# Kernel optimization log

Measured on AMD Instinct MI355X. Metric: run time of the kernel, lower is better.

## Reference

```python
import jax, jax.numpy as jnp
import numpy as np

B, L = 2, 2048
D_MODEL = 1024; D_STATE = 128; D_CONV = 4; EXPAND = 2; HEADDIM = 64
D_HALF = D_MODEL // 2
D_INNER = EXPAND * D_HALF           # 1024
NHEADS = D_INNER // HEADDIM         # 16
CONV_DIM = D_INNER + 2 * D_STATE    # 1280 (x, B, C share the depthwise conv)
D_IN_PROJ = 2 * D_INNER + 2 * D_STATE + NHEADS  # 2320 (z, xBC, dt)
EPS = 1e-5


def _rmsnorm(x, w):
    return x * jax.lax.rsqrt(jnp.mean(x * x, axis=-1, keepdims=True) + EPS) * w


def _mamba2(u, in_w, conv_w, conv_b, dt_bias, A_log, D, gnorm_w, outp_w):
    """Mamba2 block (ngroups=1, rmsnorm gated, no proj biases), u: [b,l,D_HALF]."""
    b, l, _ = u.shape
    zxbcdt = u @ in_w.T                                # [b,l,D_IN_PROJ]
    z = zxbcdt[..., :D_INNER]
    xBC = zxbcdt[..., D_INNER:D_INNER + CONV_DIM]
    dt = zxbcdt[..., D_INNER + CONV_DIM:]              # [b,l,h]
    # causal depthwise conv1d (kernel D_CONV) + silu
    xp = jnp.pad(xBC, ((0, 0), (D_CONV - 1, 0), (0, 0)))
    conv = conv_b + sum(xp[:, k:k + l, :] * conv_w[:, k] for k in range(D_CONV))
    xBC = jax.nn.silu(conv)
    x = xBC[..., :D_INNER]
    Bm = xBC[..., D_INNER:D_INNER + D_STATE]           # [b,l,n]
    Cm = xBC[..., D_INNER + D_STATE:]                  # [b,l,n]
    dt = jax.nn.softplus(dt + dt_bias)                 # [b,l,h]
    A = -jnp.exp(A_log)                                # [h]
    xh = x.reshape(b, l, NHEADS, HEADDIM)              # [b,l,h,p]
    dA = jnp.exp(dt * A)                               # [b,l,h]
    dtx = dt[..., None] * xh                           # [b,l,h,p]

    def step(h, inp):
        dA_t, dtx_t, B_t, C_t = inp
        h = dA_t[:, :, None, None] * h + jnp.einsum('bhp,bn->bhpn', dtx_t, B_t)
        return h, jnp.einsum('bhpn,bn->bhp', h, C_t)

    h0 = jnp.zeros((b, NHEADS, HEADDIM, D_STATE), u.dtype)
    xs = (jnp.moveaxis(dA, 1, 0), jnp.moveaxis(dtx, 1, 0),
          jnp.moveaxis(Bm, 1, 0), jnp.moveaxis(Cm, 1, 0))
    _, ys = jax.lax.scan(step, h0, xs)                 # ys: [l,b,h,p]
    y = jnp.moveaxis(ys, 0, 1) + xh * D[None, None, :, None]
    y = y.reshape(b, l, D_INNER) * jax.nn.silu(z)      # gate, then gated RMSNorm
    y = _rmsnorm(y, gnorm_w)
    return y @ outp_w.T                                # [b,l,D_HALF]


def _forward(x, norm_w, op_w, op_b,
             f_in_w, f_conv_w, f_conv_b, f_dt_bias, f_A_log, f_D, f_gnorm_w, f_outp_w,
             b_in_w, b_conv_w, b_conv_b, b_dt_bias, b_A_log, b_D, b_gnorm_w, b_outp_w):
    xn = _rmsnorm(x, norm_w)
    x_f, x_b = xn[..., :D_HALF], xn[..., D_HALF:]
    out_f = _mamba2(x_f, f_in_w, f_conv_w, f_conv_b, f_dt_bias, f_A_log, f_D, f_gnorm_w, f_outp_w)
    out_b = jnp.flip(
        _mamba2(jnp.flip(x_b, 1), b_in_w, b_conv_w, b_conv_b, b_dt_bias, b_A_log, b_D, b_gnorm_w, b_outp_w), 1)
    out = jnp.concatenate([out_f, out_b], axis=-1) @ op_w.T + op_b
    return x + out


def _mamba_params(key, prefix):
    k = jax.random.split(key, 5)
    return {
        prefix + 'in_w': jax.random.normal(k[0], (D_IN_PROJ, D_HALF), jnp.float32) * 0.02,
        prefix + 'conv_w': jax.random.normal(k[1], (CONV_DIM, D_CONV), jnp.float32) * 0.2,
        prefix + 'conv_b': jnp.zeros((CONV_DIM,), jnp.float32),
        prefix + 'dt_bias': jax.random.normal(k[2], (NHEADS,), jnp.float32) * 0.1,
        prefix + 'A_log': jnp.log(jax.random.uniform(k[3], (NHEADS,), jnp.float32, 1.0, 16.0)),
        prefix + 'D': jnp.ones((NHEADS,), jnp.float32),
        prefix + 'gnorm_w': jnp.ones((D_INNER,), jnp.float32),
        prefix + 'outp_w': jax.random.normal(k[4], (D_HALF, D_INNER), jnp.float32) * 0.02,
    }


def setup_inputs():
    key = jax.random.key(0)
    k = jax.random.split(key, 4)
    inp = {
        'x': jax.random.normal(k[0], (B, L, D_MODEL), jnp.float32),
        'norm_w': jnp.ones((D_MODEL,), jnp.float32),
        'op_w': jax.random.normal(k[1], (D_MODEL, D_MODEL), jnp.float32) * 0.02,
        'op_b': jnp.zeros((D_MODEL,), jnp.float32),
    }
    inp.update(_mamba_params(k[2], 'f_'))
    inp.update(_mamba_params(k[3], 'b_'))
    return inp


def reference(x, norm_w, op_w, op_b,
              f_in_w, f_conv_w, f_conv_b, f_dt_bias, f_A_log, f_D, f_gnorm_w, f_outp_w,
              b_in_w, b_conv_w, b_conv_b, b_dt_bias, b_A_log, b_D, b_gnorm_w, b_outp_w):
    return _forward(x, norm_w, op_w, op_b,
                    f_in_w, f_conv_w, f_conv_b, f_dt_bias, f_A_log, f_D, f_gnorm_w, f_outp_w,
                    b_in_w, b_conv_w, b_conv_b, b_dt_bias, b_A_log, b_D, b_gnorm_w, b_outp_w)
```

## Files before the change

### kernel.cpp

```cpp
#include <hip/hip_runtime.h>
#include <math.h>

#define L_SEQ   2048
#define NBATCH  2
#define DMODEL  1024
#define DHALF   512
#define DINNER  1024
#define DSTATE  128
#define NHEADS  16
#define HEADDIM 64
#define CONVDIM 1280
#define DINPROJ 2320
#define ROWS    4096
#define NPADIN  2432

#define QCH     64
#define NCH     (L_SEQ / QCH)

typedef __attribute__((ext_vector_type(8))) short bf16x8;
typedef __attribute__((ext_vector_type(4))) float f32x4;

union US8 { uint4 q; unsigned short s[8]; };
union US4 { uint2 q; unsigned short s[4]; };

__device__ __forceinline__ float siluf(float v){ return v / (1.f + expf(-v)); }
__device__ __forceinline__ float softplusf(float v){ return v > 20.f ? v : log1pf(expf(v)); }
__device__ __forceinline__ unsigned short f2bf(float f){
  union { float f; unsigned u; } x; x.f = f;
  unsigned r = (x.u + 0x7fffu + ((x.u >> 16) & 1u)) >> 16;
  return (unsigned short)r;
}
__device__ __forceinline__ float bf2f(unsigned short u){
  union { unsigned u; float f; } x; x.u = ((unsigned)u) << 16; return x.f;
}
__device__ __forceinline__ void gload16(const void* g, void* l){
  __builtin_amdgcn_global_load_lds((const __attribute__((address_space(1))) void*)g,
                                   (__attribute__((address_space(3))) void*)l, 16, 0, 0);
}
__device__ __forceinline__ int kx(int row){ return ((row ^ (row >> 3)) & 7) << 3; }

__device__ __forceinline__ float blockReduceSum256(float v, float* red){
  #pragma unroll
  for (int o = 32; o > 0; o >>= 1) v += __shfl_xor(v, o);
  int wid = threadIdx.x >> 6, lane = threadIdx.x & 63;
  if (lane == 0) red[wid] = v;
  __syncthreads();
  return red[0] + red[1] + red[2] + red[3];
}

__global__ void rmsnorm_split_kernel(const float* __restrict__ x, const float* __restrict__ nw,
                                     unsigned short* __restrict__ uf, unsigned short* __restrict__ ub){
  __shared__ float red[4];
  int row = blockIdx.x;
  int tid = threadIdx.x;
  float4 v4 = *(const float4*)(x + (size_t)row*DMODEL + tid*4);
  float ss = v4.x*v4.x + v4.y*v4.y + v4.z*v4.z + v4.w*v4.w;
  ss = blockReduceSum256(ss, red);
  float scale = rsqrtf(ss * (1.f/DMODEL) + 1e-5f);
  int t = row & (L_SEQ-1);
  int fliprow = (row ^ t) | (L_SEQ-1-t);
  float4 w4 = *(const float4*)(nw + tid*4);
  US4 o;
  o.s[0] = f2bf(v4.x*scale*w4.x);
  o.s[1] = f2bf(v4.y*scale*w4.y);
  o.s[2] = f2bf(v4.z*scale*w4.z);
  o.s[3] = f2bf(v4.w*scale*w4.w);
  int d = tid*4;
  if (d < DHALF) *(uint2*)&uf[(size_t)row*DHALF + d] = o.q;
  else           *(uint2*)&ub[(size_t)fliprow*DHALF + (d - DHALF)] = o.q;
}

__global__ void wconv_all_kernel(const float* __restrict__ s0, const float* __restrict__ s1,
                                 const float* __restrict__ s2, const float* __restrict__ s3,
                                 const float* __restrict__ s4,
                                 unsigned short* __restrict__ d0, unsigned short* __restrict__ d1,
                                 unsigned short* __restrict__ d2, unsigned short* __restrict__ d3,
                                 unsigned short* __restrict__ d4){
  const int S01 = NPADIN*DHALF;
  const int S23 = DHALF*DINNER;
  const int S4  = DMODEL*DMODEL;
  int idx = (blockIdx.x*256 + threadIdx.x)*4;
  const float* s; unsigned short* d; int pad_rows = 0;
  if (idx < S01){ s = s0; d = d0; pad_rows = DINPROJ; }
  else if ((idx -= S01) < S01){ s = s1; d = d1; pad_rows = DINPROJ; }
  else if ((idx -= S01) < S23){ s = s2; d = d2; }
  else if ((idx -= S23) < S23){ s = s3; d = d3; }
  else if ((idx -= S23) < S4){ s = s4; d = d4; }
  else return;
  US4 o;
  if (pad_rows && (idx >> 9) >= pad_rows){
    o.s[0] = o.s[1] = o.s[2] = o.s[3] = 0;
  } else {
    float4 v = *(const float4*)&s[idx];
    o.s[0] = f2bf(v.x); o.s[1] = f2bf(v.y); o.s[2] = f2bf(v.z); o.s[3] = f2bf(v.w);
  }
  *(uint2*)&d[idx] = o.q;
}

template<int TM>
__global__ __launch_bounds__(256) void gemm_bf16_t(
    const unsigned short* __restrict__ A0, const unsigned short* __restrict__ A1, int lda,
    const unsigned short* __restrict__ W0, const unsigned short* __restrict__ W1,
    float* __restrict__ Cf, int ldc,
    const float* __restrict__ bias, const float* __restrict__ res,
    unsigned short* __restrict__ O0a, unsigned short* __restrict__ O0b, int ld0,
    unsigned short* __restrict__ O1a, unsigned short* __restrict__ O1b, int n1, int ld1,
    float* __restrict__ O2a, float* __restrict__ O2b, int n2, int ld2,
    int coff1, int flip1,
    int M, int Nreal, int K){
  constexpr int MI = TM/32;
  __shared__ unsigned short As[2][TM*32];
  __shared__ unsigned short Bs[2][128*32];
  int bid = (blockIdx.z*gridDim.y + blockIdx.y)*gridDim.x + blockIdx.x;
  int nwg = gridDim.x*gridDim.y*gridDim.z;
  int s = bid;
  if ((nwg & 7) == 0){
    int cpx = nwg >> 3;
    s = (bid & 7)*cpx + (bid >> 3);
  }
  int bx = s % gridDim.x;
  int tmp = s / gridDim.x;
  int by = tmp % gridDim.y;
  int dir = tmp / gridDim.y;

  const unsigned short* A = dir ? A1 : A0;
  const unsigned short* W = dir ? W1 : W0;
  unsigned short* O0 = dir ? O0b : O0a;
  unsigned short* O1 = dir ? O1b : O1a;
  float* O2 = dir ? O2b : O2a;
  int coff = dir ? coff1 : 0;
  int flip = dir ? flip1 : 0;

  int bm = by*TM, bn = bx*128;
  int tid = threadIdx.x;
  int lane = tid & 63;
  int wave = tid >> 6;
  int wm = (wave >> 1) * (TM/2), wn = (wave & 1) * 64;
  int l15 = lane & 15, lhi = lane >> 4;
  f32x4 acc[MI][4];
  #pragma unroll
  for (int i = 0; i < MI; i++)
    #pragma unroll
    for (int j = 0; j < 4; j++)
      acc[i][j] = (f32x4){0.f,0.f,0.f,0.f};

  auto stage = [&](int bufi, int k0){
    #pragma unroll
    for (int f = tid; f < TM*4; f += 256){
      int row = f >> 2, c8 = (f & 3) * 8;
      gload16(A + (size_t)(bm+row)*lda + k0 + c8, &As[bufi][f*8]);
    }
    #pragma unroll
    for (int f = tid; f < 512; f += 256){
      int row = f >> 2, c8 = (f & 3) * 8;
      gload16(W + (size_t)(bn+row)*K + k0 + c8, &Bs[bufi][f*8]);
    }
  };

  stage(0, 0);
  __syncthreads();
  int cur = 0;
  for (int k0 = 0; k0 < K; k0 += 32){
    if (k0 + 32 < K) stage(cur ^ 1, k0 + 32);
    bf16x8 af[MI], bfr[4];
    #pragma unroll
    for (int i = 0; i < MI; i++)
      af[i] = *(const bf16x8*)&As[cur][(wm + i*16 + l15)*32 + lhi*8];
    #pragma unroll
    for (int j = 0; j < 4; j++)
      bfr[j] = *(const bf16x8*)&Bs[cur][(wn + j*16 + l15)*32 + lhi*8];
    #pragma unroll
    for (int i = 0; i < MI; i++)
      #pragma unroll
      for (int j = 0; j < 4; j++)
        acc[i][j] = __builtin_amdgcn_mfma_f32_16x16x32_bf16(af[i], bfr[j], acc[i][j], 0, 0, 0);
    __syncthreads();
    cur ^= 1;
  }
  #pragma unroll
  for (int i = 0; i < MI; i++){
    #pragma unroll
    for (int r = 0; r < 4; r++){
      int m = bm + wm + i*16 + lhi*4 + r;
      int mo = m;
      if (flip){ int t = m & (L_SEQ-1); mo = (m ^ t) | (L_SEQ-1-t); }
      #pragma unroll
      for (int j = 0; j < 4; j++){
        int n = bn + wn + j*16 + l15;
        if (n < Nreal){
          float v = acc[i][j][r];
          if (bias) v += bias[n];
          if (res)  v += res[(size_t)mo*ldc + coff + n];
          if (Cf)            Cf[(size_t)mo*ldc + coff + n] = v;
          else if (n < n1)   O0[(size_t)mo*ld0 + coff + n] = f2bf(v);
          else if (n < n2)   O1[(size_t)mo*ld1 + (n - n1)] = f2bf(v);
          else               O2[(size_t)mo*ld2 + (n - n2)] = v;
        }
      }
    }
  }
}

__global__ void conv_silu_kernel(const unsigned short* __restrict__ xbcf, const unsigned short* __restrict__ xbcb,
                                 const float* __restrict__ cwf, const float* __restrict__ cbf,
                                 const float* __restrict__ cwb, const float* __restrict__ cbb,
                                 unsigned short* __restrict__ cvf, unsigned short* __restrict__ cvb){
  int row = blockIdx.x;
  int tid = threadIdx.x;
  int dir = tid >= 160;
  int slot = tid - dir*160;
  const unsigned short* xbc = dir ? xbcb : xbcf;
  const float* cw = dir ? cwb : cwf;
  const float* cb = dir ? cbb : cbf;
  unsigned short* cv = dir ? cvb : cvf;
  int t = row & (L_SEQ-1);
  int c0 = slot*8;
  const unsigned short* base = xbc + (size_t)row*CONVDIM + c0;
  US8 u3, u2, u1, u0;
  u3.q = *(const uint4*)base;
  u2.q = (t >= 1) ? *(const uint4*)(base - CONVDIM)   : (uint4){0,0,0,0};
  u1.q = (t >= 2) ? *(const uint4*)(base - 2*CONVDIM) : (uint4){0,0,0,0};
  u0.q = (t >= 3) ? *(const uint4*)(base - 3*CONVDIM) : (uint4){0,0,0,0};
  US8 o;
  #pragma unroll
  for (int j = 0; j < 8; j++){
    float4 w = *(const float4*)&cw[(c0+j)*4];
    float v = cb[c0+j];
    v += bf2f(u3.s[j])*w.w + bf2f(u2.s[j])*w.z + bf2f(u1.s[j])*w.y + bf2f(u0.s[j])*w.x;
    o.s[j] = f2bf(siluf(v));
  }
  *(uint4*)&cv[(size_t)row*CONVDIM + c0] = o.q;
}

__global__ void dtcum_kernel(const float* __restrict__ drf, const float* __restrict__ drb,
                             const float* __restrict__ dbf, const float* __restrict__ alf,
                             const float* __restrict__ dbb, const float* __restrict__ alb,
                             float* __restrict__ dtf, float* __restrict__ dtb,
                             float* __restrict__ acs){
  int tid = threadIdx.x;
  int wid = blockIdx.x*4 + (tid >> 6);
  int tau = tid & 63;
  int c = wid & 31, dbh = wid >> 5;
  int h = dbh & 15, b = (dbh >> 4) & 1, dir = dbh >> 5;
  const float* dr = dir ? drb : drf;
  size_t row = (size_t)b*L_SEQ + c*QCH + tau;
  float raw = dr[row*NHEADS + h];
  float bias = (dir ? dbb : dbf)[h];
  float dtv = softplusf(raw + bias);
  float a = -expf((dir ? alb : alf)[h]);
  (dir ? dtb : dtf)[row*NHEADS + h] = dtv;
  float v = dtv * a;
  #pragma unroll
  for (int off = 1; off < 64; off <<= 1){
    float u = __shfl_up(v, off);
    if (tau >= off) v += u;
  }
  acs[(size_t)dbh*L_SEQ + c*QCH + tau] = v;
}

__global__ __launch_bounds__(256) void gemm_g_kernel(
    const unsigned short* __restrict__ cvf, const unsigned short* __restrict__ cvb,
    float* __restrict__ G){
  int c = blockIdx.x, db = blockIdx.y;
  int b = db & 1, dir = db >> 1;
  const unsigned short* cv = dir ? cvb : cvf;
  float* Gp = G + ((size_t)(db*32 + c))*4096;
  int tid = threadIdx.x, lane = tid & 63, w = tid >> 6;
  int l15 = lane & 15, lhi = lane >> 4;
  __shared__ unsigned short sB[64*128];
  __shared__ unsigned short sC[64*128];
  size_t r0 = (size_t)b*L_SEQ + (size_t)c*QCH;
  #pragma unroll
  for (int k = 0; k < 4; k++){
    int cid = k*256 + tid;
    int row = cid >> 4, slot = cid & 15;
    US8 ub, uc;
    ub.q = *(const uint4*)&cv[(r0+row)*CONVDIM + DINNER + slot*8];
    uc.q = *(const uint4*)&cv[(r0+row)*CONVDIM + DINNER + DSTATE + slot*8];
    *(uint4*)&sB[row*128 + (slot*8 ^ kx(row))] = ub.q;
    *(uint4*)&sC[row*128 + (slot*8 ^ kx(row))] = uc.q;
  }
  __syncthreads();
  int t0 = w*16;
  bf16x8 af[4];
  #pragma unroll
  for (int ks = 0; ks < 4; ks++){
    int r = t0 + l15;
    af[ks] = *(const bf16x8*)&sC[r*128 + ((ks*32 + lhi*8) ^ kx(r))];
  }
  f32x4 acc[4];
  #pragma unroll
  for (int j = 0; j < 4; j++) acc[j] = (f32x4){0.f,0.f,0.f,0.f};
  #pragma unroll
  for (int j = 0; j < 4; j++){
    #pragma unroll
    for (int ks = 0; ks < 4; ks++){
      int r = j*16 + l15;
      bf16x8 wf = *(const bf16x8*)&sB[r*128 + ((ks*32 + lhi*8) ^ kx(r))];
      acc[j] = __builtin_amdgcn_mfma_f32_16x16x32_bf16(af[ks], wf, acc[j], 0, 0, 0);
    }
  }
  #pragma unroll
  for (int j = 0; j < 4; j++)
    #pragma unroll
    for (int r = 0; r < 4; r++)
      Gp[(t0 + lhi*4 + r)*64 + j*16 + l15] = acc[j][r];
}

__global__ __launch_bounds__(256) void intra_kernel(
    const unsigned short* __restrict__ cvf, const unsigned short* __restrict__ cvb,
    const float* __restrict__ dtf, const float* __restrict__ dtb,
    const float* __restrict__ acs, const float* __restrict__ G,
    float* __restrict__ yf, float* __restrict__ yb,
    unsigned short* __restrict__ S16f, unsigned short* __restrict__ S16b){
  int c = blockIdx.x, dbh = blockIdx.y;
  int h = dbh & 15, b = (dbh >> 4) & 1, dir = dbh >> 5;
  const unsigned short* cv = dir ? cvb : cvf;
  const float* dtp = dir ? dtb : dtf;
  float* y = dir ? yb : yf;
  unsigned short* S16 = dir ? S16b : S16f;
  const float* Gp = G + ((size_t)((dir*2+b)*32 + c))*4096;
  int tid = threadIdx.x, lane = tid & 63, w = tid >> 6;
  int l15 = lane & 15, lhi = lane >> 4;

  __shared__ unsigned short sGh [64*64];
  __shared__ unsigned short sDxT[64*64];
  __shared__ unsigned short sBwT[128*64];
  __shared__ float a_sh[QCH], dt_sh[QCH];

  size_t r0 = (size_t)b*L_SEQ + (size_t)c*QCH;
  if (tid < 64){
    a_sh[tid]  = acs[(size_t)dbh*L_SEQ + c*QCH + tid];
    dt_sh[tid] = dtp[(r0 + tid)*NHEADS + h];
  }
  __syncthreads();
  float a63 = a_sh[63];
  #pragma unroll
  for (int k = 0; k < 2; k++){
    int cid = k*256 + tid;
    int s = cid >> 3, p0 = (cid & 7)*8;
    US8 u; u.q = *(const uint4*)&cv[(r0+s)*CONVDIM + h*HEADDIM + p0];
    float d = dt_sh[s];
    #pragma unroll
    for (int j = 0; j < 8; j++){
      int p = p0 + j;
      sDxT[p*64 + (s ^ kx(p))] = f2bf(bf2f(u.s[j]) * d);
    }
  }
  #pragma unroll
  for (int k = 0; k < 4; k++){
    int cid = k*256 + tid;
    int s = cid >> 4, n0 = (cid & 15)*8;
    US8 u; u.q = *(const uint4*)&cv[(r0+s)*CONVDIM + DINNER + n0];
    float wv = expf(a63 - a_sh[s]);
    #pragma unroll
    for (int j = 0; j < 8; j++){
      int n = n0 + j;
      sBwT[n*64 + (s ^ kx(n))] = f2bf(bf2f(u.s[j]) * wv);
    }
  }
  #pragma unroll
  for (int k = 0; k < 4; k++){
    int f = k*256 + tid;
    int t = f >> 4, s0 = (f & 15)*4;
    float4 g = *(const float4*)&Gp[t*64 + s0];
    float at = a_sh[t];
    float v0 = (s0+0 <= t) ? g.x*expf(at - a_sh[s0+0]) : 0.f;
    float v1 = (s0+1 <= t) ? g.y*expf(at - a_sh[s0+1]) : 0.f;
    float v2 = (s0+2 <= t) ? g.z*expf(at - a_sh[s0+2]) : 0.f;
    float v3 = (s0+3 <= t) ? g.w*expf(at - a_sh[s0+3]) : 0.f;
    int addr = t*64 + (s0 ^ kx(t));
    *(unsigned*)&sGh[addr]     = (unsigned)f2bf(v0) | ((unsigned)f2bf(v1) << 16);
    *(unsigned*)&sGh[addr + 2] = (unsigned)f2bf(v2) | ((unsigned)f2bf(v3) << 16);
  }
  __syncthreads();

  int t0 = w*16;
  bf16x8 aY[2], aS[2];
  #pragma unroll
  for (int ks = 0; ks < 2; ks++){
    int rg = t0 + l15;
    aY[ks] = *(const bf16x8*)&sGh [rg*64 + ((ks*32 + lhi*8) ^ kx(rg))];
    aS[ks] = *(const bf16x8*)&sDxT[rg*64 + ((ks*32 + lhi*8) ^ kx(rg))];
  }
  f32x4 accY[4];
  #pragma unroll
  for (int j = 0; j < 4; j++) accY[j] = (f32x4){0.f,0.f,0.f,0.f};
  #pragma unroll
  for (int j = 0; j < 4; j++){
    #pragma unroll
    for (int ks = 0; ks < 2; ks++){
      int rp = j*16 + l15;
      bf16x8 wf = *(const bf16x8*)&sDxT[rp*64 + ((ks*32 + lhi*8) ^ kx(rp))];
      accY[j] = __builtin_amdgcn_mfma_f32_16x16x32_bf16(aY[ks], wf, accY[j], 0, 0, 0);
    }
  }
  f32x4 accS[8];
  #pragma unroll
  for (int j = 0; j < 8; j++) accS[j] = (f32x4){0.f,0.f,0.f,0.f};
  #pragma unroll
  for (int j = 0; j < 8; j++){
    #pragma unroll
    for (int ks = 0; ks < 2; ks++){
      int rn = j*16 + l15;
      bf16x8 wf = *(const bf16x8*)&sBwT[rn*64 + ((ks*32 + lhi*8) ^ kx(rn))];
      accS[j] = __builtin_amdgcn_mfma_f32_16x16x32_bf16(aS[ks], wf, accS[j], 0, 0, 0);
    }
  }
  #pragma unroll
  for (int j = 0; j < 4; j++){
    #pragma unroll
    for (int r = 0; r < 4; r++){
      int t = t0 + lhi*4 + r, p = j*16 + l15;
      y[(r0 + t)*DINNER + h*HEADDIM + p] = accY[j][r];
    }
  }
  size_t sbase = ((size_t)((b*NHEADS + h)*NCH + c))*8192;
  #pragma unroll
  for (int j = 0; j < 8; j++){
    #pragma unroll
    for (int r = 0; r < 4; r++){
      int p = t0 + lhi*4 + r, n = j*16 + l15;
      S16[sbase + p*128 + n] = f2bf(accS[j][r]);
    }
  }
}

__global__ void chunkscan_kernel(const unsigned short* __restrict__ S16f,
                                 const unsigned short* __restrict__ S16b,
                                 const float* __restrict__ acs,
                                 unsigned short* __restrict__ hin16){
  __shared__ float sa[NCH];
  int tid = threadIdx.x;
  int dbh = blockIdx.x >> 4;
  int e0 = ((blockIdx.x & 15)*256 + tid)*2;
  int bh = dbh & 31, dir = dbh >> 5;
  const unsigned short* S16 = dir ? S16b : S16f;
  if (tid < NCH) sa[tid] = expf(acs[(size_t)dbh*L_SEQ + tid*QCH + 63]);
  __syncthreads();
  float h0 = 0.f, h1 = 0.f;
  #pragma unroll 8
  for (int c = 0; c < NCH; ++c){
    size_t sidx = ((size_t)(bh*NCH + c))*8192 + e0;
    size_t hidx = ((size_t)(dbh*NCH + c))*8192 + e0;
    unsigned sv = *(const unsigned*)&S16[sidx];
    unsigned hv = (unsigned)f2bf(h0) | ((unsigned)f2bf(h1) << 16);
    *(unsigned*)&hin16[hidx] = hv;
    float ea = sa[c];
    h0 = ea*h0 + bf2f((unsigned short)(sv & 0xffff));
    h1 = ea*h1 + bf2f((unsigned short)(sv >> 16));
  }
}

__global__ __launch_bounds__(256) void inter_kernel(
    const unsigned short* __restrict__ cvf, const unsigned short* __restrict__ cvb,
    const float* __restrict__ acs, const unsigned short* __restrict__ hin16,
    const float* __restrict__ Df, const float* __restrict__ Db,
    const float* __restrict__ yf, const float* __restrict__ yb,
    unsigned short* __restrict__ ygf, unsigned short* __restrict__ ygb){
  int c = blockIdx.x, dbh = blockIdx.y;
  int h = dbh & 15, b = (dbh >> 4) & 1, dir = dbh >> 5;
  const unsigned short* cv = dir ? cvb : cvf;
  const float* y = dir ? yb : yf;
  unsigned short* yg = dir ? ygb : ygf;
  float Dh = (dir ? Db : Df)[h];
  int tid = threadIdx.x, lane = tid & 63, w = tid >> 6;
  int l15 = lane & 15, lhi = lane >> 4;
  __shared__ unsigned short sC [64*128];
  __shared__ unsigned short sHT[64*128];
  __shared__ float e_sh[QCH];
  size_t r0 = (size_t)b*L_SEQ + (size_t)c*QCH;
  size_t hbase = ((size_t)(dbh*NCH + c))*8192;
  if (tid < 64) e_sh[tid] = expf(acs[(size_t)dbh*L_SEQ + c*QCH + tid]);
  #pragma unroll
  for (int k = 0; k < 4; k++){
    int cid = k*256 + tid;
    int row = cid >> 4, slot = cid & 15;
    US8 uc, uh;
    uc.q = *(const uint4*)&cv[(r0+row)*CONVDIM + DINNER + DSTATE + slot*8];
    uh.q = *(const uint4*)&hin16[hbase + cid*8];
    *(uint4*)&sC [row*128 + (slot*8 ^ kx(row))] = uc.q;
    *(uint4*)&sHT[row*128 + (slot*8 ^ kx(row))] = uh.q;
  }
  __syncthreads();
  int t0 = w*16;
  bf16x8 af[4];
  #pragma unroll
  for (int ks = 0; ks < 4; ks++){
    int r = t0 + l15;
    af[ks] = *(const bf16x8*)&sC[r*128 + ((ks*32 + lhi*8) ^ kx(r))];
  }
  f32x4 acc[4];
  #pragma unroll
  for (int j = 0; j < 4; j++) acc[j] = (f32x4){0.f,0.f,0.f,0.f};
  #pragma unroll
  for (int j = 0; j < 4; j++){
    #pragma unroll
    for (int ks = 0; ks < 4; ks++){
      int r = j*16 + l15;
      bf16x8 wf = *(const bf16x8*)&sHT[r*128 + ((ks*32 + lhi*8) ^ kx(r))];
      acc[j] = __builtin_amdgcn_mfma_f32_16x16x32_bf16(af[ks], wf, acc[j], 0, 0, 0);
    }
  }
  #pragma unroll
  for (int j = 0; j < 4; j++){
    #pragma unroll
    for (int r = 0; r < 4; r++){
      int t = t0 + lhi*4 + r, p = j*16 + l15;
      size_t row = r0 + t;
      float xv = bf2f(cv[row*CONVDIM + h*HEADDIM + p]);
      float v = y[row*DINNER + h*HEADDIM + p] + e_sh[t]*acc[j][r] + Dh*xv;
      yg[row*DINNER + h*HEADDIM + p] = f2bf(v);
    }
  }
}

__global__ void gate_norm_kernel(unsigned short* __restrict__ ygf, unsigned short* __restrict__ ygb,
                                 const unsigned short* __restrict__ z16f, const unsigned short* __restrict__ z16b,
                                 const float* __restrict__ gwf, const float* __restrict__ gwb){
  __shared__ float red[4];
  int row = blockIdx.x; int dir = blockIdx.y;
  int tid = threadIdx.x;
  unsigned short* yg = (dir ? ygb : ygf) + (size_t)row*DINNER;
  const unsigned short* z = (dir ? z16b : z16f) + (size_t)row*DINNER;
  const float* gw = dir ? gwb : gwf;
  int d = tid*4;
  US4 uy, uz;
  uy.q = *(const uint2*)&yg[d];
  uz.q = *(const uint2*)&z[d];
  float v[4]; float ss = 0.f;
  #pragma unroll
  for (int k = 0; k < 4; k++){
    float val = bf2f(uy.s[k]) * siluf(bf2f(uz.s[k]));
    v[k] = val; ss += val*val;
  }
  ss = blockReduceSum256(ss, red);
  float scale = rsqrtf(ss*(1.f/DINNER) + 1e-5f);
  float4 w4 = *(const float4*)&gw[d];
  US4 o;
  o.s[0] = f2bf(v[0]*scale*w4.x);
  o.s[1] = f2bf(v[1]*scale*w4.y);
  o.s[2] = f2bf(v[2]*scale*w4.z);
  o.s[3] = f2bf(v[3]*scale*w4.w);
  *(uint2*)&yg[d] = o.q;
}

extern "C" void kernel_launch(void* const* d_in, const int* in_sizes, int n_in,
                              void* d_out, int out_size, void* d_ws, size_t ws_size,
                              hipStream_t stream) {
  const float* x      = (const float*)d_in[0];
  const float* norm_w = (const float*)d_in[1];
  const float* op_w   = (const float*)d_in[2];
  const float* op_b   = (const float*)d_in[3];
  const float* f_in_w    = (const float*)d_in[4];
  const float* f_conv_w  = (const float*)d_in[5];
  const float* f_conv_b  = (const float*)d_in[6];
  const float* f_dt_bias = (const float*)d_in[7];
  const float* f_A_log   = (const float*)d_in[8];
  const float* f_D       = (const float*)d_in[9];
  const float* f_gnorm_w = (const float*)d_in[10];
  const float* f_outp_w  = (const float*)d_in[11];
  const float* b_in_w    = (const float*)d_in[12];
  const float* b_conv_w  = (const float*)d_in[13];
  const float* b_conv_b  = (const float*)d_in[14];
  const float* b_dt_bias = (const float*)d_in[15];
  const float* b_A_log   = (const float*)d_in[16];
  const float* b_D       = (const float*)d_in[17];
  const float* b_gnorm_w = (const float*)d_in[18];
  const float* b_outp_w  = (const float*)d_in[19];
  float* out = (float*)d_out;

  float* ws = (float*)d_ws;
  size_t off = 0;
  unsigned short* u16f = (unsigned short*)(ws + off);
  unsigned short* u16b = u16f + (size_t)ROWS*DHALF;      off += (size_t)ROWS*DHALF;
  unsigned short* z16f = (unsigned short*)(ws + off);    off += (size_t)ROWS*DINNER/2;
  unsigned short* z16b = (unsigned short*)(ws + off);    off += (size_t)ROWS*DINNER/2;
  unsigned short* xbc16f = (unsigned short*)(ws + off);  off += (size_t)ROWS*CONVDIM/2;
  unsigned short* xbc16b = (unsigned short*)(ws + off);  off += (size_t)ROWS*CONVDIM/2;
  float* draw_f = ws + off; off += (size_t)ROWS*NHEADS;
  float* draw_b = ws + off; off += (size_t)ROWS*NHEADS;
  unsigned short* cv16f = (unsigned short*)(ws + off); off += (size_t)ROWS*CONVDIM/2;
  unsigned short* cv16b = (unsigned short*)(ws + off); off += (size_t)ROWS*CONVDIM/2;
  float* dt_f = ws + off; off += (size_t)ROWS*NHEADS;
  float* dt_b = ws + off; off += (size_t)ROWS*NHEADS;
  float* y_f  = ws + off; off += (size_t)ROWS*DINNER;
  float* y_b  = ws + off; off += (size_t)ROWS*DINNER;
  unsigned short* yg16f = (unsigned short*)(ws + off); off += (size_t)ROWS*DINNER/2;
  unsigned short* yg16b = (unsigned short*)(ws + off); off += (size_t)ROWS*DINNER/2;
  float* acs  = ws + off; off += (size_t)64*L_SEQ;
  float* G    = ws + off; off += (size_t)128*QCH*QCH;
  unsigned short* S16f = (unsigned short*)(ws + off); off += (size_t)32*NCH*8192/2;
  unsigned short* S16b = (unsigned short*)(ws + off); off += (size_t)32*NCH*8192/2;
  unsigned short* hin16 = (unsigned short*)(ws + off); off += (size_t)64*NCH*8192/2;
  unsigned short* w16_fin  = (unsigned short*)(ws + off); off += (size_t)NPADIN*DHALF/2;
  unsigned short* w16_bin  = (unsigned short*)(ws + off); off += (size_t)NPADIN*DHALF/2;
  unsigned short* w16_fout = (unsigned short*)(ws + off); off += (size_t)DHALF*DINNER/2;
  unsigned short* w16_bout = (unsigned short*)(ws + off); off += (size_t)DHALF*DINNER/2;
  unsigned short* w16_op   = (unsigned short*)(ws + off); off += (size_t)DMODEL*DMODEL/2;
  unsigned short* cat16 = z16f;

  rmsnorm_split_kernel<<<ROWS, 256, 0, stream>>>(x, norm_w, u16f, u16b);
  {
    const int TOT = 2*NPADIN*DHALF + 2*DHALF*DINNER + DMODEL*DMODEL;
    wconv_all_kernel<<<(TOT/4+255)/256, 256, 0, stream>>>(
        f_in_w, b_in_w, f_outp_w, b_outp_w, op_w,
        w16_fin, w16_bin, w16_fout, w16_bout, w16_op);
  }
  gemm_bf16_t<128><<<dim3(NPADIN/128, ROWS/128, 2), 256, 0, stream>>>(
      u16f, u16b, DHALF, w16_fin, w16_bin,
      nullptr, 0, nullptr, nullptr,
      z16f, z16b, DINNER,
      xbc16f, xbc16b, DINNER, CONVDIM,
      draw_f, draw_b, DINNER+CONVDIM, NHEADS,
      0, 0,
      ROWS, DINPROJ, DHALF);
  conv_silu_kernel<<<ROWS, 320, 0, stream>>>(
      xbc16f, xbc16b, f_conv_w, f_conv_b, b_conv_w, b_conv_b, cv16f, cv16b);
  dtcum_kernel<<<512, 256, 0, stream>>>(
      draw_f, draw_b, f_dt_bias, f_A_log, b_dt_bias, b_A_log, dt_f, dt_b, acs);
  gemm_g_kernel<<<dim3(32, 4), 256, 0, stream>>>(cv16f, cv16b, G);
  intra_kernel<<<dim3(32, 64), 256, 0, stream>>>(cv16f, cv16b, dt_f, dt_b, acs, G,
                                                 y_f, y_b, S16f, S16b);
  chunkscan_kernel<<<1024, 256, 0, stream>>>(S16f, S16b, acs, hin16);
  inter_kernel<<<dim3(32, 64), 256, 0, stream>>>(cv16f, cv16b, acs, hin16, f_D, b_D,
                                                 y_f, y_b, yg16f, yg16b);
  gate_norm_kernel<<<dim3(ROWS, 2), 256, 0, stream>>>(
      yg16f, yg16b, z16f, z16b, f_gnorm_w, b_gnorm_w);
  gemm_bf16_t<64><<<dim3(DHALF/128, ROWS/64, 2), 256, 0, stream>>>(
      yg16f, yg16b, DINNER, w16_fout, w16_bout,
      nullptr, 0, nullptr, nullptr,
      cat16, cat16, DMODEL,
      nullptr, nullptr, 1<<30, 0,
      nullptr, nullptr, 1<<30, 0,
      DHALF, 1,
      ROWS, DHALF, DINNER);
  gemm_bf16_t<64><<<dim3(DMODEL/128, ROWS/64, 1), 256, 0, stream>>>(
      cat16, nullptr, DMODEL, w16_op, nullptr,
      out, DMODEL, op_b, x,
      nullptr, nullptr, 0,
      nullptr, nullptr, 1<<30, 0,
      nullptr, nullptr, 1<<30, 0,
      0, 0,
      ROWS, DMODEL, DMODEL);
}
```

Before: 222.8 us.

## Triple-buffer GEMM LDS staging with vmcnt waits and XOR bank swizzle

The bf16 GEMM moves from double to triple buffering of its LDS tiles. It issues loads two k-steps ahead and uses explicit s_waitcnt vmcnt counts plus raw s_barrier in place of __syncthreads, so global loads overlap more MFMA work. It also XOR-swizzles the 16-byte chunk position per row to cut LDS bank conflicts on the fragment reads. The cost is 50% more LDS per block, which may reduce occupancy, and the hand-counted vmcnt values depend on exactly P loads per stage.

Result: faster. 215.8 us (-3.1%).

```diff
diff --git a/kernel.cpp b/kernel.cpp
--- a/kernel.cpp
+++ b/kernel.cpp
@@ -38,6 +38,7 @@
                                    (__attribute__((address_space(3))) void*)l, 16, 0, 0);
 }
 __device__ __forceinline__ int kx(int row){ return ((row ^ (row >> 3)) & 7) << 3; }
+__device__ __forceinline__ int sw4(int row){ return (row ^ (row >> 2)) & 3; }
 
 __device__ __forceinline__ float blockReduceSum256(float v, float* red){
   #pragma unroll
@@ -109,8 +110,9 @@
     int coff1, int flip1,
     int M, int Nreal, int K){
   constexpr int MI = TM/32;
-  __shared__ unsigned short As[2][TM*32];
-  __shared__ unsigned short Bs[2][128*32];
+  constexpr int P = TM/64 + 2;
+  __shared__ unsigned short As[3][TM*32];
+  __shared__ unsigned short Bs[3][128*32];
   int bid = (blockIdx.z*gridDim.y + blockIdx.y)*gridDim.x + blockIdx.x;
   int nwg = gridDim.x*gridDim.y*gridDim.z;
   int s = bid;
@@ -144,38 +146,52 @@
     for (int j = 0; j < 4; j++)
       acc[i][j] = (f32x4){0.f,0.f,0.f,0.f};
 
-  auto stage = [&](int bufi, int k0){
+  auto stage = [&](int sl, int k0){
     #pragma unroll
     for (int f = tid; f < TM*4; f += 256){
-      int row = f >> 2, c8 = (f & 3) * 8;
-      gload16(A + (size_t)(bm+row)*lda + k0 + c8, &As[bufi][f*8]);
+      int row = f >> 2, c = (f & 3) ^ sw4(row);
+      gload16(A + (size_t)(bm+row)*lda + k0 + c*8, &As[sl][f*8]);
     }
     #pragma unroll
     for (int f = tid; f < 512; f += 256){
-      int row = f >> 2, c8 = (f & 3) * 8;
-      gload16(W + (size_t)(bn+row)*K + k0 + c8, &Bs[bufi][f*8]);
+      int row = f >> 2, c = (f & 3) ^ sw4(row);
+      gload16(W + (size_t)(bn+row)*K + k0 + c*8, &Bs[sl][f*8]);
     }
   };
 
+  int NK = K >> 5;
   stage(0, 0);
-  __syncthreads();
-  int cur = 0;
-  for (int k0 = 0; k0 < K; k0 += 32){
-    if (k0 + 32 < K) stage(cur ^ 1, k0 + 32);
+  if (NK > 1) stage(1, 32);
+  int sl = 0;
+  for (int it = 0; it < NK; ++it){
+    if (it + 2 < NK){
+      int s2 = sl + 2; if (s2 >= 3) s2 -= 3;
+      stage(s2, (it + 2) << 5);
+      asm volatile("s_waitcnt vmcnt(%0)" :: "n"(2*P) : "memory");
+    } else if (it + 1 < NK){
+      asm volatile("s_waitcnt vmcnt(%0)" :: "n"(P) : "memory");
+    } else {
+      asm volatile("s_waitcnt vmcnt(0)" ::: "memory");
+    }
+    asm volatile("s_barrier" ::: "memory");
     bf16x8 af[MI], bfr[4];
     #pragma unroll
-    for (int i = 0; i < MI; i++)
-      af[i] = *(const bf16x8*)&As[cur][(wm + i*16 + l15)*32 + lhi*8];
-    #pragma unroll
-    for (int j = 0; j < 4; j++)
-      bfr[j] = *(const bf16x8*)&Bs[cur][(wn + j*16 + l15)*32 + lhi*8];
+    for (int i = 0; i < MI; i++){
+      int r = wm + i*16 + l15;
+      af[i] = *(const bf16x8*)&As[sl][(r*4 + (lhi ^ sw4(r)))*8];
+    }
+    #pragma unroll
+    for (int j = 0; j < 4; j++){
+      int r = wn + j*16 + l15;
+      bfr[j] = *(const bf16x8*)&Bs[sl][(r*4 + (lhi ^ sw4(r)))*8];
+    }
     #pragma unroll
     for (int i = 0; i < MI; i++)
       #pragma unroll
       for (int j = 0; j < 4; j++)
         acc[i][j] = __builtin_amdgcn_mfma_f32_16x16x32_bf16(af[i], bfr[j], acc[i][j], 0, 0, 0);
-    __syncthreads();
-    cur ^= 1;
+    asm volatile("s_barrier" ::: "memory");
+    sl = (sl + 1 == 3) ? 0 : sl + 1;
   }
   #pragma unroll
   for (int i = 0; i < MI; i++){
```
